# Kernel tuning notes

Hardware: AMD Instinct MI355X
Metric: run time of the kernel (lower is better)

## Reference

```python
import jax, jax.numpy as jnp
import numpy as np

D_MODEL = 1024
N_HEAD = 16
D_HEAD = D_MODEL // N_HEAD
FFN_HIDDEN = 4096
NEG_INF = -1e30


def sinusoid_pos_emb(pos_seq, d_model):
    # pos_seq: [K] descending relative positions; returns [K, d_model]
    inv_freq = 1.0 / (10000.0 ** (jnp.arange(0, d_model, 2, dtype=jnp.float32) / d_model))
    ang = pos_seq[:, None] * inv_freq[None, :]
    return jnp.concatenate([jnp.sin(ang), jnp.cos(ang)], axis=-1)


def rel_shift(x):
    # x: [B, H, Q, K] -> Transformer-XL relative shift
    b, h, q, k = x.shape
    x = jnp.pad(x, ((0, 0), (0, 0), (0, 0), (1, 0)))
    x = x.reshape(b, h, k + 1, q)[:, :, 1:, :].reshape(b, h, q, k)
    return x


def layer_norm(x, g, b, eps=1e-5):
    mu = jnp.mean(x, axis=-1, keepdims=True)
    var = jnp.var(x, axis=-1, keepdims=True)
    return (x - mu) * jax.lax.rsqrt(var + eps) * g + b


def setup_inputs() -> dict:
    key = jax.random.key(0)
    ks = jax.random.split(key, 20)
    B, T, M = 4, 2048, 2048
    s = 0.02
    inp = {
        "x": jax.random.normal(ks[0], (B, T, D_MODEL), jnp.float32),
        "mem": jax.random.normal(ks[1], (B, M, D_MODEL), jnp.float32),
        "Wq": jax.random.normal(ks[2], (D_MODEL, D_MODEL), jnp.float32) * s,
        "bq": jnp.zeros((D_MODEL,), jnp.float32),
        "Wk": jax.random.normal(ks[3], (D_MODEL, D_MODEL), jnp.float32) * s,
        "bk": jnp.zeros((D_MODEL,), jnp.float32),
        "Wv": jax.random.normal(ks[4], (D_MODEL, D_MODEL), jnp.float32) * s,
        "bv": jnp.zeros((D_MODEL,), jnp.float32),
        "Wo": jax.random.normal(ks[5], (D_MODEL, D_MODEL), jnp.float32) * s,
        "bo": jnp.zeros((D_MODEL,), jnp.float32),
        "Wr": jax.random.normal(ks[6], (D_MODEL, D_MODEL), jnp.float32) * s,
        "u": jax.random.normal(ks[7], (N_HEAD, D_HEAD), jnp.float32) * s,
        "v": jax.random.normal(ks[8], (N_HEAD, D_HEAD), jnp.float32) * s,
        "g1": jnp.ones((D_MODEL,), jnp.float32),
        "be1": jnp.zeros((D_MODEL,), jnp.float32),
        "g2": jnp.ones((D_MODEL,), jnp.float32),
        "be2": jnp.zeros((D_MODEL,), jnp.float32),
        "W1": jax.random.normal(ks[9], (D_MODEL, FFN_HIDDEN), jnp.float32) * s,
        "b1": jnp.zeros((FFN_HIDDEN,), jnp.float32),
        "W2": jax.random.normal(ks[10], (FFN_HIDDEN, D_MODEL), jnp.float32) * s,
        "b2": jnp.zeros((D_MODEL,), jnp.float32),
        "is_causal": 1,
    }
    return inp


def xl_attention(x, mem, Wq, bq, Wk, bk, Wv, bv, Wo, bo, Wr, u, v, is_causal):
    B, T, D = x.shape
    M = mem.shape[1]
    K = M + T
    c = jnp.concatenate([mem, x], axis=1)  # [B, K, D]
    q = (x @ Wq + bq).reshape(B, T, N_HEAD, D_HEAD)
    k = (c @ Wk + bk).reshape(B, K, N_HEAD, D_HEAD)
    vv = (c @ Wv + bv).reshape(B, K, N_HEAD, D_HEAD)
    pos_seq = jnp.arange(K - 1, -1, -1, dtype=jnp.float32)
    r = (sinusoid_pos_emb(pos_seq, D) @ Wr).reshape(K, N_HEAD, D_HEAD)
    # content term + relative-position term (Transformer-XL eq. A+C and B+D)
    AC = jnp.einsum('bihd,bjhd->bhij', q + u, k)
    BD = rel_shift(jnp.einsum('bihd,jhd->bhij', q + v, r))
    score = (AC + BD) * (1.0 / np.sqrt(D_HEAD))
    if is_causal:
        i = jnp.arange(T)[:, None]
        j = jnp.arange(K)[None, :]
        causal = (j <= i + M)  # query i may attend keys up to its own position
        score = jnp.where(causal[None, None], score, NEG_INF)
    attn = jax.nn.softmax(score, axis=-1)
    out = jnp.einsum('bhij,bjhd->bihd', attn, vv).reshape(B, T, D)
    return out @ Wo + bo


def reference(x, mem, Wq, bq, Wk, bk, Wv, bv, Wo, bo, Wr, u, v,
              g1, be1, g2, be2, W1, b1, W2, b2, is_causal):
    # dropout is identity at inference
    a = xl_attention(x, mem, Wq, bq, Wk, bk, Wv, bv, Wo, bo, Wr, u, v, is_causal)
    h = layer_norm(a + x, g1, be1)
    f = jax.nn.gelu(h @ W1 + b1) @ W2 + b2
    return layer_norm(f + h, g2, be2)
```

## Files before the change

kernel.cpp:

```cpp
#include <hip/hip_runtime.h>
#include <stdint.h>

typedef unsigned short u16;
typedef short s16x8 __attribute__((ext_vector_type(8)));
typedef unsigned short u16x4 __attribute__((ext_vector_type(4)));
typedef float f32x4 __attribute__((ext_vector_type(4)));

#define DEV static __device__ __forceinline__

DEV u16 f2b(float f) {
  union { float f; unsigned u; } v; v.f = f;
  unsigned r = v.u + 0x7fffu + ((v.u >> 16) & 1u);
  return (u16)(r >> 16);
}
DEV float b2f(u16 b) {
  union { unsigned u; float f; } v; v.u = ((unsigned)b) << 16; return v.f;
}
DEV unsigned pk_trunc(float a, float b) {
  return __builtin_amdgcn_perm(__float_as_uint(b), __float_as_uint(a), 0x07060302u);
}
DEV f32x4 MFMA16(s16x8 a, s16x8 b, f32x4 c) {
  return __builtin_amdgcn_mfma_f32_16x16x32_bf16(a, b, c, 0, 0, 0);
}
#define GLD_LDS16(gp, lp)                                                            \
  __builtin_amdgcn_global_load_lds((const __attribute__((address_space(1))) void*)(gp), \
                                   (__attribute__((address_space(3))) void*)(lp), 16, 0, 0)


__global__ __launch_bounds__(256) void wt_cast_t(const float* __restrict__ W,
                                                 u16* __restrict__ Wt, int Kd, int Nd) {
  __shared__ float tile[32][33];
  const int n0 = blockIdx.x * 32, k0 = blockIdx.y * 32;
  const int t = threadIdx.x;
#pragma unroll
  for (int p = 0; p < 4; ++p) {
    int idx = p * 256 + t; int r = idx >> 5, c = idx & 31;
    tile[r][c] = W[(long)(k0 + r) * Nd + n0 + c];
  }
  __syncthreads();
#pragma unroll
  for (int p = 0; p < 4; ++p) {
    int idx = p * 256 + t; int r = idx >> 5, c = idx & 31;
    Wt[(long)(n0 + r) * Kd + k0 + c] = f2b(tile[c][r]);
  }
}

__global__ __launch_bounds__(256) void build_cb(const float* __restrict__ x,
                                                const float* __restrict__ mem,
                                                u16* __restrict__ cb) {
  long idx = (long)blockIdx.x * 256 + threadIdx.x;
  long e4 = idx * 4;
  int b = (int)(e4 >> 22);
  long rem = e4 & ((1L << 22) - 1);
  int tok = (int)(rem >> 10);
  int d = (int)(rem & 1023);
  const float* src = (tok < 2048) ? &mem[((long)b * 2048 + tok) * 1024 + d]
                                  : &x[((long)b * 2048 + (tok - 2048)) * 1024 + d];
  float4 vv = *(const float4*)src;
  uint2 o;
  o.x = (unsigned)f2b(vv.x) | ((unsigned)f2b(vv.y) << 16);
  o.y = (unsigned)f2b(vv.z) | ((unsigned)f2b(vv.w) << 16);
  *(uint2*)&cb[e4] = o;
}

__global__ __launch_bounds__(256) void pos_emb(u16* __restrict__ pe) {
  const int d = blockIdx.x;
  const int e0 = threadIdx.x * 4;
  u16 o[4];
#pragma unroll
  for (int i = 0; i < 4; ++i) {
    int e = e0 + i;
    int f = (e < 512) ? e : (e - 512);
    float invf = expf(-(float)f * (9.210340371976184f / 512.f));
    float ang = (float)d * invf;
    o[i] = f2b((e < 512) ? sinf(ang) : cosf(ang));
  }
  uint2 pk; pk.x = (unsigned)o[0] | ((unsigned)o[1] << 16);
  pk.y = (unsigned)o[2] | ((unsigned)o[3] << 16);
  *(uint2*)&pe[(long)d * 1024 + e0] = pk;
}

#define EPI_BF16 0
#define EPI_F32 1
#define EPI_GELU 2
#define EPI_VT 3

template <int EPI, int QMAP>
__global__ __launch_bounds__(256) void gemm_bt(const u16* __restrict__ A,
                                               const u16* __restrict__ Bt,
                                               const float* __restrict__ bias,
                                               void* __restrict__ outp, int Ndim, int Kdim) {
  __shared__ __align__(16) u16 As[128 * 64];
  __shared__ __align__(16) u16 Bs[128 * 64];
  const int col0 = blockIdx.x * 128;
  const int row0 = blockIdx.y * 128;
  const int t = threadIdx.x;
  const int w = t >> 6, l = t & 63;
  const int wr = (w >> 1) * 64, wc = (w & 1) * 64;
  const int lr = l & 15, g = l >> 4;
  f32x4 acc[4][4];
#pragma unroll
  for (int m = 0; m < 4; ++m)
#pragma unroll
    for (int n = 0; n < 4; ++n) acc[m][n] = f32x4{0.f, 0.f, 0.f, 0.f};

  for (int k0 = 0; k0 < Kdim; k0 += 64) {
#pragma unroll
    for (int it = 0; it < 4; ++it) {
      int c = it * 256 + t;
      int r = c >> 3, ch = (c & 7) ^ (r & 7);
      long ga = row0 + r;
      if (QMAP) ga = ((ga >> 11) << 12) + 2048 + (ga & 2047);
      GLD_LDS16(A + ga * Kdim + k0 + ch * 8, &As[c * 8]);
      GLD_LDS16(Bt + (long)(col0 + r) * Kdim + k0 + ch * 8, &Bs[c * 8]);
    }
    __syncthreads();
#pragma unroll
    for (int kk = 0; kk < 2; ++kk) {
      s16x8 af[4], bfv[4];
#pragma unroll
      for (int m = 0; m < 4; ++m) {
        int rm = wr + m * 16 + lr;
        af[m] = *(const s16x8*)&As[rm * 64 + (((g + 4 * kk) ^ (rm & 7)) << 3)];
      }
#pragma unroll
      for (int n = 0; n < 4; ++n) {
        int rn = wc + n * 16 + lr;
        bfv[n] = *(const s16x8*)&Bs[rn * 64 + (((g + 4 * kk) ^ (rn & 7)) << 3)];
      }
#pragma unroll
      for (int m = 0; m < 4; ++m)
#pragma unroll
        for (int n = 0; n < 4; ++n) acc[m][n] = MFMA16(af[m], bfv[n], acc[m][n]);
    }
    __syncthreads();
  }

  const int lg = g * 4;
#pragma unroll
  for (int m = 0; m < 4; ++m) {
    int rbase = row0 + wr + m * 16 + lg;
#pragma unroll
    for (int n = 0; n < 4; ++n) {
      int gc = col0 + wc + n * 16 + lr;
      float bv = bias ? bias[gc] : 0.f;
#pragma unroll
      for (int rg = 0; rg < 4; ++rg) {
        float vv = acc[m][n][rg] + bv;
        ((u16*)outp)[(long)(rbase + rg) * Ndim + gc] = f2b(vv);
      }
    }
  }
}

template <int EPI, int QMAP, int BN>
__global__ __launch_bounds__(512) void gemm_big(const u16* __restrict__ A,
                                                const u16* __restrict__ Bt,
                                                const float* __restrict__ bias,
                                                void* __restrict__ outp, int Ndim, int Kdim) {
  constexpr int NF = BN / 64;
  __shared__ __align__(16) u16 As[2][256 * 64];
  __shared__ __align__(16) u16 Bs[2][BN * 64];
  const int col0 = blockIdx.x * BN;
  const int row0 = blockIdx.y * 256;
  const int t = threadIdx.x;
  const int w = t >> 6, l = t & 63;
  const int wr = (w >> 2) * 128, wc = (w & 3) * (BN / 4);
  const int lr = l & 15, g = l >> 4;

  f32x4 acc[8][NF];
#pragma unroll
  for (int m = 0; m < 8; ++m)
#pragma unroll
    for (int n = 0; n < NF; ++n) acc[m][n] = f32x4{0.f, 0.f, 0.f, 0.f};

  auto stageA = [&](int k0, int p, int nb) {
    int c = p * 512 + t;
    int r = c >> 3, ch = (c & 7) ^ (r & 7);
    long ga = row0 + r;
    if (QMAP) ga = ((ga >> 11) << 12) + 2048 + (ga & 2047);
    GLD_LDS16(A + ga * Kdim + k0 + ch * 8, &As[nb][c * 8]);
  };
  auto stageB = [&](int k0, int p, int nb) {
    int c = p * 512 + t;
    int r = c >> 3, ch = (c & 7) ^ (r & 7);
    GLD_LDS16(Bt + (long)(col0 + r) * Kdim + k0 + ch * 8, &Bs[nb][c * 8]);
  };

  const int nt = Kdim >> 6;
#pragma unroll
  for (int p = 0; p < 4; ++p) stageA(0, p, 0);
#pragma unroll
  for (int p = 0; p < NF; ++p) stageB(0, p, 0);
  __syncthreads();
  int cur = 0;

  for (int ti = 0; ti < nt; ++ti) {
    const int k1 = (ti + 1) << 6;
    const int nb = cur ^ 1;
    s16x8 bf[NF][2];
#pragma unroll
    for (int p = 0; p < 4; ++p) {
      s16x8 af[2][2];
#pragma unroll
      for (int i = 0; i < 2; ++i) {
        int rm = wr + (2 * p + i) * 16 + lr;
#pragma unroll
        for (int kk = 0; kk < 2; ++kk)
          af[i][kk] = *(const s16x8*)&As[cur][rm * 64 + (((g + 4 * kk) ^ (rm & 7)) << 3)];
      }
      if (p == 0) {
#pragma unroll
        for (int n = 0; n < NF; ++n) {
          int rn = wc + n * 16 + lr;
#pragma unroll
          for (int kk = 0; kk < 2; ++kk)
            bf[n][kk] = *(const s16x8*)&Bs[cur][rn * 64 + (((g + 4 * kk) ^ (rn & 7)) << 3)];
        }
      }
      if (ti + 1 < nt) {
        if (p == 0) { stageA(k1, 0, nb); stageB(k1, 0, nb); }
        else if (p == 1) { stageA(k1, 1, nb); if (NF > 1) stageB(k1, 1, nb); }
        else if (p == 2) {
          stageA(k1, 2, nb); stageA(k1, 3, nb);
          if (NF == 4) { stageB(k1, 2, nb); stageB(k1, 3, nb); }
        }
      }
      __builtin_amdgcn_s_barrier();
      __builtin_amdgcn_s_setprio(1);
#pragma unroll
      for (int i = 0; i < 2; ++i)
#pragma unroll
        for (int n = 0; n < NF; ++n) {
          acc[2 * p + i][n] = MFMA16(af[i][0], bf[n][0], acc[2 * p + i][n]);
          acc[2 * p + i][n] = MFMA16(af[i][1], bf[n][1], acc[2 * p + i][n]);
        }
      __builtin_amdgcn_s_setprio(0);
      if (p < 3) __builtin_amdgcn_s_barrier();
    }
    __syncthreads();
    cur ^= 1;
  }

  const int lg = g * 4;
#pragma unroll
  for (int m = 0; m < 8; ++m) {
    int rbase = row0 + wr + m * 16 + lg;
#pragma unroll
    for (int n = 0; n < NF; ++n) {
      int gc = col0 + wc + n * 16 + lr;
      float bv = bias ? bias[gc] : 0.f;
#pragma unroll
      for (int rg = 0; rg < 4; ++rg) {
        int grow = rbase + rg;
        float vv = acc[m][n][rg] + bv;
        if (EPI == EPI_GELU) {
          float x3 = vv * vv * vv;
          vv = 0.5f * vv * (1.f + tanhf(0.7978845608028654f * (vv + 0.044715f * x3)));
        }
        if (EPI == EPI_F32) {
          ((float*)outp)[(long)grow * Ndim + gc] = vv;
        } else if (EPI == EPI_VT) {
          int bb = grow >> 12, tok = grow & 4095;
          int hh = gc >> 6, dd = gc & 63;
          ((u16*)outp)[((long)((bb * 16 + hh) * 64 + dd) << 12) + tok] = f2b(vv);
        } else {
          ((u16*)outp)[(long)grow * Ndim + gc] = f2b(vv);
        }
      }
    }
  }
}

#define SCALE_LOG2 0.18033688011111793f

__global__ __launch_bounds__(1024, 4) void attn_fused(
    const u16* __restrict__ qg, const u16* __restrict__ kg, const u16* __restrict__ vTg,
    const u16* __restrict__ rg, const float* __restrict__ u, const float* __restrict__ vparam,
    const int* __restrict__ causal_p, u16* __restrict__ Og) {
  __shared__ __align__(16) u16 Ks[2][128 * 64];
  __shared__ __align__(16) u16 Vs[2][128 * 64];
  __shared__ __align__(16) u16 GPs[16][16 * 84];

  const int bh = blockIdx.x, b = bh >> 4, h = bh & 15;
  const int i0 = (int)(gridDim.y - 1 - blockIdx.y) * 256;
  const int t = threadIdx.x, w = t >> 6, l = t & 63;
  const int q = l & 15, g = l >> 4, lk = g * 8;
  const int causal = causal_p[0];

  const long kbase = ((long)b * 4096) * 1024 + h * 64;
  const long vbase = ((long)((b * 16 + h) * 64)) * 4096;

  const int irow = i0 + 16 * w + q;
  const u16* qp = qg + ((long)(b * 2048 + irow)) * 1024 + h * 64;
  s16x8 qlo = *(const s16x8*)(qp + lk);
  s16x8 qhi = *(const s16x8*)(qp + 32 + lk);
  s16x8 qu0, qu1, qv0, qv1;
#pragma unroll
  for (int j = 0; j < 8; ++j) {
    float a0 = b2f((u16)qlo[j]), a1 = b2f((u16)qhi[j]);
    float uu0 = u[h * 64 + lk + j], vv0 = vparam[h * 64 + lk + j];
    float uu1 = u[h * 64 + 32 + lk + j], vv1 = vparam[h * 64 + 32 + lk + j];
    qu0[j] = (short)f2b((a0 + uu0) * SCALE_LOG2); qv0[j] = (short)f2b((a0 + vv0) * SCALE_LOG2);
    qu1[j] = (short)f2b((a1 + uu1) * SCALE_LOG2); qv1[j] = (short)f2b((a1 + vv1) * SCALE_LOG2);
  }

  float lsum = 0.f;
  f32x4 oacc[4];
#pragma unroll
  for (int n = 0; n < 4; ++n) oacc[n] = f32x4{0.f, 0.f, 0.f, 0.f};

  u16* gpw = &GPs[w][0];
  const int kc0 = q * 64 + ((g ^ (q & 7)) << 3);
  const int kc1 = kc0 ^ 32;
  const int gq = q * 85 + 63;
  const int gst = q * 84 + 4 * g;
  const int pst = q * 72 + 4 * g;
  const int prd = q * 72 + lk;

  auto STAGE = [&](int j0s, int bufi) {
    {
      int rrow = t >> 3, ch = (t & 7) ^ (rrow & 7);
      GLD_LDS16(kg + kbase + (long)(j0s + rrow) * 1024 + ch * 8, &Ks[bufi][t * 8]);
    }
    {
      int s = t >> 9, c9 = t & 511;
      int rrow = c9 >> 3, ch = (c9 & 7) ^ (rrow & 7);
      GLD_LDS16(vTg + vbase + (long)rrow * 4096 + j0s + s * 64 + ch * 8,
                &Vs[bufi][(s << 12) + c9 * 8]);
    }
  };

  s16x8 rf0[5], rf1[5];
  auto LOADR = [&](int j0r) {
    const int dlo = 2048 + i0 + 16 * w - j0r - 63;
#pragma unroll
    for (int tt = 0; tt < 5; ++tt) {
      int d = dlo + tt * 16 + q; d = min(max(d, 0), 4095);
      const u16* rp = rg + ((long)d << 10) + h * 64;
      rf0[tt] = *(const s16x8*)(rp + lk);
      rf1[tt] = *(const s16x8*)(rp + 32 + lk);
    }
  };

  const int jmaxB = causal ? (2048 + i0 + 256) : 4096;
  const int NT = jmaxB >> 7;
  const int jlimit = 2048 + i0 + 16 * w + 15;

  STAGE(0, 0);
  LOADR(0);
  int cur = 0;

  for (int TI = 0; TI < NT; ++TI) {
    __syncthreads();
    if (TI + 1 < NT) STAGE((TI + 1) << 7, cur ^ 1);

#pragma unroll
    for (int s = 0; s < 2; ++s) {
      const int j0 = (TI << 7) + (s << 6);
      if (!causal || j0 <= jlimit) {
        const u16* ksp = &Ks[cur][s << 12];
        const u16* vsp = &Vs[cur][s << 12];

        f32x4 sv[4];
        __builtin_amdgcn_s_setprio(1);
#pragma unroll
        for (int n = 0; n < 4; ++n) {
          s16x8 af0 = *(const s16x8*)&ksp[kc0 + n * 1024];
          s16x8 af1 = *(const s16x8*)&ksp[kc1 + n * 1024];
          f32x4 z = f32x4{0.f, 0.f, 0.f, 0.f};
          z = MFMA16(af0, qu0, z);
          z = MFMA16(af1, qu1, z);
          sv[n] = z;
        }
#pragma unroll
        for (int tt = 0; tt < 5; ++tt) {
          f32x4 z = f32x4{0.f, 0.f, 0.f, 0.f};
          z = MFMA16(rf0[tt], qv0, z);
          z = MFMA16(rf1[tt], qv1, z);
          uint2 gp2 = {pk_trunc(z[0], z[1]), pk_trunc(z[2], z[3])};
          *(u16x4*)&gpw[gst + tt * 16] = __builtin_bit_cast(u16x4, gp2);
        }
        __builtin_amdgcn_s_setprio(0);

        if (j0 + 64 < jmaxB && (!causal || j0 + 64 <= jlimit)) LOADR(j0 + 64);

        const bool need_mask = (causal != 0) && (j0 + 63 > 2048 + i0 + 16 * w);
#pragma unroll
        for (int n = 0; n < 4; ++n) {
#pragma unroll
          for (int r = 0; r < 4; ++r) {
            int j = 16 * n + 4 * g + r;
            float bd = b2f(gpw[gq - j]);
            float scv = sv[n][r] + bd;
            if (need_mask && (j0 + j > 2048 + irow)) scv = -3.0e38f;
            sv[n][r] = scv;
          }
        }
        float ls = 0.f;
#pragma unroll
        for (int n = 0; n < 4; ++n) {
          float p0 = __builtin_amdgcn_exp2f(sv[n][0]);
          float p1 = __builtin_amdgcn_exp2f(sv[n][1]);
          float p2 = __builtin_amdgcn_exp2f(sv[n][2]);
          float p3 = __builtin_amdgcn_exp2f(sv[n][3]);
          ls += (p0 + p1) + (p2 + p3);
          uint2 pp = {pk_trunc(p0, p1), pk_trunc(p2, p3)};
          *(u16x4*)&gpw[pst + n * 16] = __builtin_bit_cast(u16x4, pp);
        }
        lsum += ls;

        s16x8 pb0 = *(const s16x8*)&gpw[prd];
        s16x8 pb1 = *(const s16x8*)&gpw[prd + 32];
        __builtin_amdgcn_s_setprio(1);
#pragma unroll
        for (int n = 0; n < 4; ++n) {
          s16x8 va0 = *(const s16x8*)&vsp[kc0 + n * 1024];
          s16x8 va1 = *(const s16x8*)&vsp[kc1 + n * 1024];
          oacc[n] = MFMA16(va0, pb0, oacc[n]);
          oacc[n] = MFMA16(va1, pb1, oacc[n]);
        }
        __builtin_amdgcn_s_setprio(0);
      }
    }
    cur ^= 1;
  }

  lsum += __shfl_xor(lsum, 16);
  lsum += __shfl_xor(lsum, 32);
  const float linv = 1.f / lsum;
  const long obase = (long)(b * 2048 + irow) * 1024 + h * 64;
#pragma unroll
  for (int n = 0; n < 4; ++n) {
    u16x4 ov = {f2b(oacc[n][0] * linv), f2b(oacc[n][1] * linv),
                f2b(oacc[n][2] * linv), f2b(oacc[n][3] * linv)};
    *(u16x4*)&Og[obase + n * 16 + 4 * g] = ov;
  }
}

template <int WRITE_BF16>
__global__ __launch_bounds__(256) void ln_res(const float* __restrict__ a,
                                              const float* __restrict__ resid,
                                              const float* __restrict__ g,
                                              const float* __restrict__ be,
                                              float* __restrict__ outf, u16* __restrict__ outb) {
  const int row = blockIdx.x;
  const int t = threadIdx.x;
  const long base = (long)row * 1024;
  float4 av = *(const float4*)&a[base + t * 4];
  float4 rv = *(const float4*)&resid[base + t * 4];
  float x0 = av.x + rv.x, x1 = av.y + rv.y, x2 = av.z + rv.z, x3 = av.w + rv.w;
  float s = x0 + x1 + x2 + x3;
  float q = x0 * x0 + x1 * x1 + x2 * x2 + x3 * x3;
#pragma unroll
  for (int d = 1; d < 64; d <<= 1) {
    s += __shfl_xor(s, d);
    q += __shfl_xor(q, d);
  }
  __shared__ float ss[4], sq[4];
  if ((t & 63) == 0) { ss[t >> 6] = s; sq[t >> 6] = q; }
  __syncthreads();
  s = ss[0] + ss[1] + ss[2] + ss[3];
  q = sq[0] + sq[1] + sq[2] + sq[3];
  float mu = s * (1.f / 1024.f);
  float var = q * (1.f / 1024.f) - mu * mu;
  float rstd = rsqrtf(var + 1e-5f);
  float4 gv = *(const float4*)&g[t * 4];
  float4 bv = *(const float4*)&be[t * 4];
  float y0 = (x0 - mu) * rstd * gv.x + bv.x;
  float y1 = (x1 - mu) * rstd * gv.y + bv.y;
  float y2 = (x2 - mu) * rstd * gv.z + bv.z;
  float y3 = (x3 - mu) * rstd * gv.w + bv.w;
  float4 ov = {y0, y1, y2, y3};
  *(float4*)&outf[base + t * 4] = ov;
  if (WRITE_BF16) {
    uint2 o;
    o.x = (unsigned)f2b(y0) | ((unsigned)f2b(y1) << 16);
    o.y = (unsigned)f2b(y2) | ((unsigned)f2b(y3) << 16);
    *(uint2*)&outb[base + t * 4] = o;
  }
}

extern "C" void kernel_launch(void* const* d_in, const int* in_sizes, int n_in, void* d_out,
                              int out_size, void* d_ws, size_t ws_size, hipStream_t stream) {
  const float* x = (const float*)d_in[0];
  const float* mem = (const float*)d_in[1];
  const float* Wq = (const float*)d_in[2];
  const float* bq = (const float*)d_in[3];
  const float* Wk = (const float*)d_in[4];
  const float* bk = (const float*)d_in[5];
  const float* Wv = (const float*)d_in[6];
  const float* bv = (const float*)d_in[7];
  const float* Wo = (const float*)d_in[8];
  const float* bo = (const float*)d_in[9];
  const float* Wr = (const float*)d_in[10];
  const float* u = (const float*)d_in[11];
  const float* vp = (const float*)d_in[12];
  const float* g1 = (const float*)d_in[13];
  const float* be1 = (const float*)d_in[14];
  const float* g2 = (const float*)d_in[15];
  const float* be2 = (const float*)d_in[16];
  const float* W1 = (const float*)d_in[17];
  const float* b1 = (const float*)d_in[18];
  const float* W2 = (const float*)d_in[19];
  const float* b2 = (const float*)d_in[20];
  const int* iscaus = (const int*)d_in[21];

  char* ws = (char*)d_ws;
  const size_t MB = 1024 * 1024;
  u16* WqT = (u16*)(ws + 0 * MB);
  u16* WkT = (u16*)(ws + 2 * MB);
  u16* WvT = (u16*)(ws + 4 * MB);
  u16* WoT = (u16*)(ws + 6 * MB);
  u16* WrT = (u16*)(ws + 8 * MB);
  u16* W1T = (u16*)(ws + 10 * MB);
  u16* W2T = (u16*)(ws + 18 * MB);
  u16* cb = (u16*)(ws + 26 * MB);
  float* proj = (float*)(ws + 26 * MB);
  u16* pe = (u16*)(ws + 58 * MB);
  u16* qb = (u16*)(ws + 66 * MB);
  u16* kb = (u16*)(ws + 82 * MB);
  u16* vT = (u16*)(ws + 114 * MB);
  u16* rb = (u16*)(ws + 146 * MB);
  u16* aO = (u16*)(ws + 154 * MB);
  u16* hb = (u16*)(ws + 154 * MB);
  u16* f1 = (u16*)(ws + 58 * MB);
  float* f2 = (float*)(ws + 122 * MB);
  (void)ws_size; (void)in_sizes; (void)n_in; (void)out_size;

  wt_cast_t<<<dim3(32, 32), 256, 0, stream>>>(Wq, WqT, 1024, 1024);
  wt_cast_t<<<dim3(32, 32), 256, 0, stream>>>(Wk, WkT, 1024, 1024);
  wt_cast_t<<<dim3(32, 32), 256, 0, stream>>>(Wv, WvT, 1024, 1024);
  wt_cast_t<<<dim3(32, 32), 256, 0, stream>>>(Wo, WoT, 1024, 1024);
  wt_cast_t<<<dim3(32, 32), 256, 0, stream>>>(Wr, WrT, 1024, 1024);
  wt_cast_t<<<dim3(128, 32), 256, 0, stream>>>(W1, W1T, 1024, 4096);
  wt_cast_t<<<dim3(32, 128), 256, 0, stream>>>(W2, W2T, 4096, 1024);

  build_cb<<<16384, 256, 0, stream>>>(x, mem, cb);
  pos_emb<<<4096, 256, 0, stream>>>(pe);

  gemm_big<EPI_BF16, 1, 128><<<dim3(8, 32), 512, 0, stream>>>(cb, WqT, bq, qb, 1024, 1024);
  gemm_big<EPI_BF16, 0, 256><<<dim3(4, 64), 512, 0, stream>>>(cb, WkT, bk, kb, 1024, 1024);
  gemm_big<EPI_VT, 0, 256><<<dim3(4, 64), 512, 0, stream>>>(cb, WvT, bv, vT, 1024, 1024);
  gemm_bt<EPI_BF16, 0><<<dim3(8, 32), 256, 0, stream>>>(pe, WrT, nullptr, rb, 1024, 1024);

  attn_fused<<<dim3(64, 8), 1024, 0, stream>>>(qb, kb, vT, rb, u, vp, iscaus, aO);

  gemm_big<EPI_F32, 0, 128><<<dim3(8, 32), 512, 0, stream>>>(aO, WoT, bo, proj, 1024, 1024);
  ln_res<1><<<8192, 256, 0, stream>>>(proj, x, g1, be1, proj, hb);

  gemm_big<EPI_GELU, 0, 256><<<dim3(16, 32), 512, 0, stream>>>(hb, W1T, b1, f1, 4096, 1024);
  gemm_big<EPI_F32, 0, 128><<<dim3(8, 32), 512, 0, stream>>>(f1, W2T, b2, f2, 1024, 4096);
  ln_res<0><<<8192, 256, 0, stream>>>(f2, proj, g2, be2, (float*)d_out, nullptr);
}
```

Before: 907.8 us.

## Interleave the two 64-key subtiles to overlap QK MFMAs with softmax

Splits the attention inner loop body into QK, positional-product, gather/softmax and PV stages, then software-pipelines the two 64-key subtiles of each 128-key block. The second subtile's QK MFMAs and positional product are issued around the first subtile's gather and exp work, so matrix and vector instructions can overlap. The positional-row prefetch for the next block moves earlier. This keeps two score fragments live at once, which raises register pressure and could hurt occupancy.

```diff
diff --git a/kernel.cpp b/kernel.cpp
--- a/kernel.cpp
+++ b/kernel.cpp
@@ -342,6 +342,70 @@
       rf1[tt] = *(const s16x8*)(rp + 32 + lk);
     }
   };
+  auto ACQK = [&](const u16* ksp, f32x4 sv[4]) {
+    __builtin_amdgcn_s_setprio(1);
+#pragma unroll
+    for (int n = 0; n < 4; ++n) {
+      s16x8 af0 = *(const s16x8*)&ksp[kc0 + n * 1024];
+      s16x8 af1 = *(const s16x8*)&ksp[kc1 + n * 1024];
+      f32x4 z = f32x4{0.f, 0.f, 0.f, 0.f};
+      z = MFMA16(af0, qu0, z);
+      z = MFMA16(af1, qu1, z);
+      sv[n] = z;
+    }
+    __builtin_amdgcn_s_setprio(0);
+  };
+  auto GPROD = [&]() {
+    __builtin_amdgcn_s_setprio(1);
+#pragma unroll
+    for (int tt = 0; tt < 5; ++tt) {
+      f32x4 z = f32x4{0.f, 0.f, 0.f, 0.f};
+      z = MFMA16(rf0[tt], qv0, z);
+      z = MFMA16(rf1[tt], qv1, z);
+      uint2 gp2 = {pk_trunc(z[0], z[1]), pk_trunc(z[2], z[3])};
+      *(u16x4*)&gpw[gst + tt * 16] = __builtin_bit_cast(u16x4, gp2);
+    }
+    __builtin_amdgcn_s_setprio(0);
+  };
+  auto GATHER_SM = [&](f32x4 sv[4], int j0s) {
+    const bool need_mask = (causal != 0) && (j0s + 63 > 2048 + i0 + 16 * w);
+#pragma unroll
+    for (int n = 0; n < 4; ++n) {
+#pragma unroll
+      for (int r = 0; r < 4; ++r) {
+        int j = 16 * n + 4 * g + r;
+        float bd = b2f(gpw[gq - j]);
+        float scv = sv[n][r] + bd;
+        if (need_mask && (j0s + j > 2048 + irow)) scv = -3.0e38f;
+        sv[n][r] = scv;
+      }
+    }
+    float ls = 0.f;
+#pragma unroll
+    for (int n = 0; n < 4; ++n) {
+      float p0 = __builtin_amdgcn_exp2f(sv[n][0]);
+      float p1 = __builtin_amdgcn_exp2f(sv[n][1]);
+      float p2 = __builtin_amdgcn_exp2f(sv[n][2]);
+      float p3 = __builtin_amdgcn_exp2f(sv[n][3]);
+      ls += (p0 + p1) + (p2 + p3);
+      uint2 pp = {pk_trunc(p0, p1), pk_trunc(p2, p3)};
+      *(u16x4*)&gpw[pst + n * 16] = __builtin_bit_cast(u16x4, pp);
+    }
+    lsum += ls;
+  };
+  auto PV = [&](const u16* vsp) {
+    s16x8 pb0 = *(const s16x8*)&gpw[prd];
+    s16x8 pb1 = *(const s16x8*)&gpw[prd + 32];
+    __builtin_amdgcn_s_setprio(1);
+#pragma unroll
+    for (int n = 0; n < 4; ++n) {
+      s16x8 va0 = *(const s16x8*)&vsp[kc0 + n * 1024];
+      s16x8 va1 = *(const s16x8*)&vsp[kc1 + n * 1024];
+      oacc[n] = MFMA16(va0, pb0, oacc[n]);
+      oacc[n] = MFMA16(va1, pb1, oacc[n]);
+    }
+    __builtin_amdgcn_s_setprio(0);
+  };
 
   const int jmaxB = causal ? (2048 + i0 + 256) : 4096;
   const int NT = jmaxB >> 7;
@@ -355,73 +419,32 @@
     __syncthreads();
     if (TI + 1 < NT) STAGE((TI + 1) << 7, cur ^ 1);
 
-#pragma unroll
-    for (int s = 0; s < 2; ++s) {
-      const int j0 = (TI << 7) + (s << 6);
-      if (!causal || j0 <= jlimit) {
-        const u16* ksp = &Ks[cur][s << 12];
-        const u16* vsp = &Vs[cur][s << 12];
-
-        f32x4 sv[4];
-        __builtin_amdgcn_s_setprio(1);
-#pragma unroll
-        for (int n = 0; n < 4; ++n) {
-          s16x8 af0 = *(const s16x8*)&ksp[kc0 + n * 1024];
-          s16x8 af1 = *(const s16x8*)&ksp[kc1 + n * 1024];
-          f32x4 z = f32x4{0.f, 0.f, 0.f, 0.f};
-          z = MFMA16(af0, qu0, z);
-          z = MFMA16(af1, qu1, z);
-          sv[n] = z;
-        }
-#pragma unroll
-        for (int tt = 0; tt < 5; ++tt) {
-          f32x4 z = f32x4{0.f, 0.f, 0.f, 0.f};
-          z = MFMA16(rf0[tt], qv0, z);
-          z = MFMA16(rf1[tt], qv1, z);
-          uint2 gp2 = {pk_trunc(z[0], z[1]), pk_trunc(z[2], z[3])};
-          *(u16x4*)&gpw[gst + tt * 16] = __builtin_bit_cast(u16x4, gp2);
-        }
-        __builtin_amdgcn_s_setprio(0);
-
-        if (j0 + 64 < jmaxB && (!causal || j0 + 64 <= jlimit)) LOADR(j0 + 64);
-
-        const bool need_mask = (causal != 0) && (j0 + 63 > 2048 + i0 + 16 * w);
-#pragma unroll
-        for (int n = 0; n < 4; ++n) {
-#pragma unroll
-          for (int r = 0; r < 4; ++r) {
-            int j = 16 * n + 4 * g + r;
-            float bd = b2f(gpw[gq - j]);
-            float scv = sv[n][r] + bd;
-            if (need_mask && (j0 + j > 2048 + irow)) scv = -3.0e38f;
-            sv[n][r] = scv;
-          }
-        }
-        float ls = 0.f;
-#pragma unroll
-        for (int n = 0; n < 4; ++n) {
-          float p0 = __builtin_amdgcn_exp2f(sv[n][0]);
-          float p1 = __builtin_amdgcn_exp2f(sv[n][1]);
-          float p2 = __builtin_amdgcn_exp2f(sv[n][2]);
-          float p3 = __builtin_amdgcn_exp2f(sv[n][3]);
-          ls += (p0 + p1) + (p2 + p3);
-          uint2 pp = {pk_trunc(p0, p1), pk_trunc(p2, p3)};
-          *(u16x4*)&gpw[pst + n * 16] = __builtin_bit_cast(u16x4, pp);
-        }
-        lsum += ls;
-
-        s16x8 pb0 = *(const s16x8*)&gpw[prd];
-        s16x8 pb1 = *(const s16x8*)&gpw[prd + 32];
-        __builtin_amdgcn_s_setprio(1);
-#pragma unroll
-        for (int n = 0; n < 4; ++n) {
-          s16x8 va0 = *(const s16x8*)&vsp[kc0 + n * 1024];
-          s16x8 va1 = *(const s16x8*)&vsp[kc1 + n * 1024];
-          oacc[n] = MFMA16(va0, pb0, oacc[n]);
-          oacc[n] = MFMA16(va1, pb1, oacc[n]);
-        }
-        __builtin_amdgcn_s_setprio(0);
-      }
+    const int j0 = TI << 7, j1 = j0 + 64;
+    const bool l0 = !causal || j0 <= jlimit;
+    const bool l1 = !causal || j1 <= jlimit;
+    const u16* ksp0 = &Ks[cur][0];
+    const u16* vsp0 = &Vs[cur][0];
+    const u16* ksp1 = &Ks[cur][4096];
+    const u16* vsp1 = &Vs[cur][4096];
+
+    if (l1) {
+      f32x4 sv0[4], sv1[4];
+      ACQK(ksp0, sv0);
+      GPROD();
+      LOADR(j1);
+      ACQK(ksp1, sv1);
+      GATHER_SM(sv0, j0);
+      GPROD();
+      PV(vsp0);
+      if (TI + 1 < NT) LOADR(j0 + 128);
+      GATHER_SM(sv1, j1);
+      PV(vsp1);
+    } else if (l0) {
+      f32x4 sv0[4];
+      ACQK(ksp0, sv0);
+      GPROD();
+      GATHER_SM(sv0, j0);
+      PV(vsp0);
     }
     cur ^= 1;
   }
```

After: 1.300 ms. 43.2% more time.
